# Kernel tuning notes

Measured on AMD Instinct MI355X. Metric: run time of the kernel, lower is better.

The kernel has to match this reference:

```python
import jax, jax.numpy as jnp
import numpy as np

E = 64          # num experts
CAP = 64        # tokens per expert (uniform routing)
H = 1024        # hidden_size
F = 2048        # ffn_hidden_size


def setup_inputs() -> dict:
    key = jax.random.key(0)
    k1, k2, k3 = jax.random.split(key, 3)
    x = jax.random.normal(k1, (E * CAP, H), dtype=jnp.float32)
    # dMoE stores expert weights flattened as [E*F, H]
    w1 = jax.random.normal(k2, (E * F, H), dtype=jnp.float32) * 0.02
    w2 = jax.random.normal(k3, (E * F, H), dtype=jnp.float32) * 0.02
    return {"x": x, "w1": w1, "w2": w2, "num_experts": E}


def reference(x, w1, w2, num_experts):
    # Block-sparse sdd/dsd over a block-diagonal expert topology is a grouped GEMM:
    # tokens are sorted by expert; each group of CAP tokens hits one expert's weights.
    T, Hd = x.shape
    Fd = w1.shape[0] // num_experts
    cap = T // num_experts
    xg = x.reshape(num_experts, cap, Hd)            # [E, cap, H]
    w1g = w1.reshape(num_experts, Fd, Hd)           # [E, F, H]
    w2g = w2.reshape(num_experts, Fd, Hd)           # [E, F, H]
    # sdd: x @ w1^T restricted to expert blocks
    h = jnp.einsum('ech,efh->ecf', xg, w1g)         # [E, cap, F]
    # megablocks' gelu kernel uses the tanh approximation
    h = jax.nn.gelu(h, approximate=True)
    # dsd: h @ w2 restricted to expert blocks
    out = jnp.einsum('ecf,efh->ech', h, w2g)        # [E, cap, H]
    return out.reshape(T, Hd)
```

## Files before the change

### kernel.cpp

```cpp
#include <hip/hip_runtime.h>


typedef __attribute__((ext_vector_type(8))) short short8;
typedef __attribute__((ext_vector_type(4))) float f32x4;
typedef __attribute__((ext_vector_type(8))) unsigned short ushort8;

#define NE   64
#define CAPT 64
#define HD   1024
#define FD   2048

__device__ __forceinline__ unsigned short f2bf(float f) {
  union { float f; unsigned u; } v; v.f = f;
  unsigned r = v.u + 0x7FFFu + ((v.u >> 16) & 1u);
  return (unsigned short)(r >> 16);
}

__device__ __forceinline__ float gelu_t(float v) {
  float u = 1.5957691216057308f * (v + 0.044715f * v * v * v);
  return v / (1.0f + __expf(-u));
}

__device__ __forceinline__ int swz(int row, int kbyte) {
  return row * 128 + (kbyte ^ ((row & 7) << 4));
}
__device__ __forceinline__ int swz2(int row, int kbyte) {
  return row * 256 + (kbyte ^ ((row & 7) << 4));
}

__device__ __forceinline__ void cvt_wr4(unsigned char* dst, f32x4 v) {
  uint2 p;
  p.x = (unsigned)f2bf(v.x) | ((unsigned)f2bf(v.y) << 16);
  p.y = (unsigned)f2bf(v.z) | ((unsigned)f2bf(v.w) << 16);
  *(uint2*)dst = p;
}

__device__ __forceinline__ void tile_barrier() {
  asm volatile("s_waitcnt lgkmcnt(0)" ::: "memory");
  __builtin_amdgcn_s_barrier();
  __builtin_amdgcn_sched_barrier(0);
}

__device__ __forceinline__ int xcd_swz(int bid, int grid) {
  return (bid & 7) * (grid >> 3) + (bid >> 3);
}

#define P1_TSZ (64 * 256)
__global__ __launch_bounds__(512, 4)
void moe_pass1(const float* __restrict__ x, const float* __restrict__ w1,
               unsigned short* __restrict__ hb) {
  __shared__ __align__(16) unsigned char sA[2 * P1_TSZ];
  __shared__ __align__(16) unsigned char sB[2 * P1_TSZ];
  const int bid = xcd_swz(blockIdx.x, NE * 32);
  const int e = bid >> 5, nb = bid & 31;
  const int t = threadIdx.x, lane = t & 63, wid = t >> 6;
  const int wm = wid >> 2, wn = wid & 3;
  const int lr = lane & 15, lk16 = (lane >> 4) * 16;

  const float* xg  = x  + (size_t)e * CAPT * HD;
  const float* w1g = w1 + ((size_t)e * FD + (size_t)nb * 64) * HD;

  f32x4 acc[2] = {};

  f32x4 ra0[4], ra1[4], rb0[4], rb1[4];
  auto loadA = [&](f32x4 (&ra)[4], int k0) {
    #pragma unroll
    for (int i = 0; i < 4; ++i) {
      int u = t + i * 512;
      ra[i] = *(const f32x4*)(xg + (u >> 5) * HD + k0 + (u & 31) * 4);
    }
  };
  auto loadB = [&](f32x4 (&rb)[4], int k0) {
    #pragma unroll
    for (int i = 0; i < 4; ++i) {
      int u = t + i * 512;
      rb[i] = __builtin_nontemporal_load(
          (const f32x4*)(w1g + (u >> 5) * HD + k0 + (u & 31) * 4));
    }
  };
  auto writeT = [&](unsigned char* a, unsigned char* b,
                    f32x4 (&ra)[4], f32x4 (&rb)[4]) {
    #pragma unroll
    for (int i = 0; i < 4; ++i) {
      int u = t + i * 512;
      cvt_wr4(a + swz2(u >> 5, (u & 31) * 8), ra[i]);
    }
    #pragma unroll
    for (int i = 0; i < 4; ++i) {
      int u = t + i * 512;
      cvt_wr4(b + swz2(u >> 5, (u & 31) * 8), rb[i]);
    }
  };

  const int NK = HD / 128;
  loadA(ra0, 0);   loadB(rb0, 0);
  writeT(sA, sB, ra0, rb0);
  loadA(ra1, 128); loadB(rb1, 128);
  loadA(ra0, 256); loadB(rb0, 256);
  tile_barrier();

  int cur = 0;
  auto step = [&](int ks, f32x4 (&raS)[4], f32x4 (&rbS)[4]) {
    unsigned char* cA = sA + cur * P1_TSZ;
    unsigned char* cB = sB + cur * P1_TSZ;
    if (ks + 1 < NK) writeT(sA + (cur ^ 1) * P1_TSZ, sB + (cur ^ 1) * P1_TSZ,
                            raS, rbS);
    if (ks + 3 < NK) { loadA(raS, (ks + 3) * 128); loadB(rbS, (ks + 3) * 128); }

    #pragma unroll
    for (int kk = 0; kk < 4; ++kk) {
      short8 af0 = *(const short8*)(cA + swz2(wm * 32 + lr,      kk * 64 + lk16));
      short8 af1 = *(const short8*)(cA + swz2(wm * 32 + 16 + lr, kk * 64 + lk16));
      short8 bfr = *(const short8*)(cB + swz2(wn * 16 + lr,      kk * 64 + lk16));
      acc[0] = __builtin_amdgcn_mfma_f32_16x16x32_bf16(af0, bfr, acc[0], 0, 0, 0);
      acc[1] = __builtin_amdgcn_mfma_f32_16x16x32_bf16(af1, bfr, acc[1], 0, 0, 0);
    }
    tile_barrier();
    cur ^= 1;
  };
  #pragma unroll 1
  for (int ks = 0; ks < NK; ks += 2) {
    step(ks,     ra1, rb1);
    step(ks + 1, ra0, rb0);
  }

  unsigned short* hp = hb + (size_t)e * CAPT * FD + nb * 64;
  #pragma unroll
  for (int fm = 0; fm < 2; ++fm)
    #pragma unroll
    for (int j = 0; j < 4; ++j) {
      int m = wm * 32 + fm * 16 + (lane >> 4) * 4 + j;
      int f = wn * 16 + lr;
      hp[(size_t)m * FD + f] = f2bf(gelu_t(acc[fm][j]));
    }
}

#define A_SZ (64 * 128)
#define B_SZ (128 * 128)

__global__ __launch_bounds__(512, 4)
void moe_pass2(const unsigned short* __restrict__ hb, const float* __restrict__ w2,
               float* __restrict__ out) {
  __shared__ __align__(16) unsigned char sA[2 * A_SZ];
  __shared__ __align__(16) unsigned char sB[2 * B_SZ];
  const int bid = xcd_swz(blockIdx.x, NE * 8);
  const int e = bid >> 3, nb = bid & 7;
  const int t = threadIdx.x, lane = t & 63, wid = t >> 6;
  const int wm = wid >> 2, wn = wid & 3;
  const int lr = lane & 15, lkb = (lane >> 4) * 16;

  const unsigned short* hg = hb + (size_t)e * CAPT * FD;
  const float* w2g = w2 + (size_t)e * FD * HD + nb * 128;

  f32x4 acc[2][2] = {};

  const int ar = t >> 3, ac = t & 7;
  const int bn = t & 127, bkg = t >> 7;

  ushort8 rav0, rav1;
  float rbv0[16], rbv1[16];
  auto loadA = [&](ushort8& rav, int f0) {
    rav = *(const ushort8*)(hg + (size_t)ar * FD + f0 + ac * 8);
  };
  auto loadB = [&](float (&rbv)[16], int f0) {
    #pragma unroll
    for (int i = 0; i < 4; ++i)
      #pragma unroll
      for (int j = 0; j < 4; ++j)
        rbv[i * 4 + j] = __builtin_nontemporal_load(
            w2g + (size_t)(f0 + bkg * 16 + i * 4 + j) * HD + bn);
  };
  auto writeT = [&](unsigned char* a, unsigned char* b,
                    ushort8& rav, float (&rbv)[16]) {
    *(ushort8*)(a + swz(ar, ac * 16)) = rav;
    #pragma unroll
    for (int i = 0; i < 4; ++i) {
      uint2 p;
      p.x = (unsigned)f2bf(rbv[i * 4 + 0]) | ((unsigned)f2bf(rbv[i * 4 + 1]) << 16);
      p.y = (unsigned)f2bf(rbv[i * 4 + 2]) | ((unsigned)f2bf(rbv[i * 4 + 3]) << 16);
      *(uint2*)(b + swz(bn, (bkg * 16 + i * 4) * 2)) = p;
    }
  };

  const int NK = FD / 64;
  loadA(rav0, 0);   loadB(rbv0, 0);
  writeT(sA, sB, rav0, rbv0);
  loadA(rav1, 64);  loadB(rbv1, 64);
  loadA(rav0, 128); loadB(rbv0, 128);
  tile_barrier();

  int cur = 0;
  auto step = [&](int ks, ushort8& ravS, float (&rbvS)[16]) {
    unsigned char* cA = sA + cur * A_SZ;
    unsigned char* cB = sB + cur * B_SZ;
    if (ks + 1 < NK) writeT(sA + (cur ^ 1) * A_SZ, sB + (cur ^ 1) * B_SZ,
                            ravS, rbvS);
    if (ks + 3 < NK) { loadA(ravS, (ks + 3) * 64); loadB(rbvS, (ks + 3) * 64); }

    short8 af[2][2], bf[2][2];
    #pragma unroll
    for (int fm = 0; fm < 2; ++fm)
      #pragma unroll
      for (int kk = 0; kk < 2; ++kk)
        af[fm][kk] = *(const short8*)(cA + swz(wm * 32 + fm * 16 + lr, kk * 64 + lkb));
    #pragma unroll
    for (int fn = 0; fn < 2; ++fn)
      #pragma unroll
      for (int kk = 0; kk < 2; ++kk)
        bf[fn][kk] = *(const short8*)(cB + swz(wn * 32 + fn * 16 + lr, kk * 64 + lkb));
    #pragma unroll
    for (int fm = 0; fm < 2; ++fm)
      #pragma unroll
      for (int fn = 0; fn < 2; ++fn) {
        acc[fm][fn] = __builtin_amdgcn_mfma_f32_16x16x32_bf16(af[fm][0], bf[fn][0], acc[fm][fn], 0, 0, 0);
        acc[fm][fn] = __builtin_amdgcn_mfma_f32_16x16x32_bf16(af[fm][1], bf[fn][1], acc[fm][fn], 0, 0, 0);
      }
    tile_barrier();
    cur ^= 1;
  };
  #pragma unroll 1
  for (int ks = 0; ks < NK; ks += 2) {
    step(ks,     rav1, rbv1);
    step(ks + 1, rav0, rbv0);
  }

  float* op = out + (size_t)e * CAPT * HD + nb * 128;
  #pragma unroll
  for (int fm = 0; fm < 2; ++fm)
    #pragma unroll
    for (int fn = 0; fn < 2; ++fn)
      #pragma unroll
      for (int j = 0; j < 4; ++j) {
        int m = wm * 32 + fm * 16 + (lane >> 4) * 4 + j;
        int n = wn * 32 + fn * 16 + lr;
        __builtin_nontemporal_store(acc[fm][fn][j], op + (size_t)m * HD + n);
      }
}

extern "C" void kernel_launch(void* const* d_in, const int* in_sizes, int n_in,
                              void* d_out, int out_size, void* d_ws, size_t ws_size,
                              hipStream_t stream) {
  const float* x  = (const float*)d_in[0];
  const float* w1 = (const float*)d_in[1];
  const float* w2 = (const float*)d_in[2];
  float* out = (float*)d_out;
  unsigned short* hb = (unsigned short*)d_ws;
  (void)in_sizes; (void)n_in; (void)out_size; (void)ws_size;

  moe_pass1<<<dim3(NE * (FD / 64)), dim3(512), 0, stream>>>(x, w1, hb);
  moe_pass2<<<dim3(NE * (HD / 128)), dim3(512), 0, stream>>>(hb, w2, out);
}
```

Baseline: 205.7 us.

## Restructure pass1: keep expert x tile in LDS, stream w1 directly into MFMA registers

Pass1 now launches one block per expert quarter (512 F columns). Each block converts the whole 64x1024 x tile to bf16 once into a 128KB LDS buffer. Each wave then loads its own 64 rows of w1 straight from global memory into registers, packs them with v_cvt_pk_bf16_f32, and feeds them to the MFMAs as B fragments, so weights never pass through LDS and the per-step barriers are gone. This removes the repeated x reloads across 32 blocks per expert and the LDS round trip for weights. The cost is a much smaller grid (256 blocks), higher LDS and register use per block, and uncoalesced per-lane w1 loads.

```diff
diff --git a/kernel.cpp b/kernel.cpp
--- a/kernel.cpp
+++ b/kernel.cpp
@@ -3,6 +3,7 @@
 
 typedef __attribute__((ext_vector_type(8))) short short8;
 typedef __attribute__((ext_vector_type(4))) float f32x4;
+typedef __attribute__((ext_vector_type(4))) unsigned int uint4v;
 typedef __attribute__((ext_vector_type(8))) unsigned short ushort8;
 
 #define NE   64
@@ -21,11 +22,19 @@
   return v / (1.0f + __expf(-u));
 }
 
+__device__ __forceinline__ short8 pack_bf16x8(f32x4 a, f32x4 b) {
+  union { uint4v u; short8 s; } r;
+  unsigned d0, d1, d2, d3;
+  asm("v_cvt_pk_bf16_f32 %0,%1,%2" : "=v"(d0) : "v"(a.x), "v"(a.y));
+  asm("v_cvt_pk_bf16_f32 %0,%1,%2" : "=v"(d1) : "v"(a.z), "v"(a.w));
+  asm("v_cvt_pk_bf16_f32 %0,%1,%2" : "=v"(d2) : "v"(b.x), "v"(b.y));
+  asm("v_cvt_pk_bf16_f32 %0,%1,%2" : "=v"(d3) : "v"(b.z), "v"(b.w));
+  r.u.x = d0; r.u.y = d1; r.u.z = d2; r.u.w = d3;
+  return r.s;
+}
+
 __device__ __forceinline__ int swz(int row, int kbyte) {
   return row * 128 + (kbyte ^ ((row & 7) << 4));
-}
-__device__ __forceinline__ int swz2(int row, int kbyte) {
-  return row * 256 + (kbyte ^ ((row & 7) << 4));
 }
 
 __device__ __forceinline__ void cvt_wr4(unsigned char* dst, f32x4 v) {
@@ -45,94 +54,76 @@
   return (bid & 7) * (grid >> 3) + (bid >> 3);
 }
 
-#define P1_TSZ (64 * 256)
-__global__ __launch_bounds__(512, 4)
+__global__ __launch_bounds__(512, 2)
 void moe_pass1(const float* __restrict__ x, const float* __restrict__ w1,
                unsigned short* __restrict__ hb) {
-  __shared__ __align__(16) unsigned char sA[2 * P1_TSZ];
-  __shared__ __align__(16) unsigned char sB[2 * P1_TSZ];
-  const int bid = xcd_swz(blockIdx.x, NE * 32);
-  const int e = bid >> 5, nb = bid & 31;
+  __shared__ __align__(16) unsigned char sX[64 * 2048];
+  const int sb = xcd_swz(blockIdx.x, NE * 4);
+  const int e = sb >> 2, slice = sb & 3;
   const int t = threadIdx.x, lane = t & 63, wid = t >> 6;
-  const int wm = wid >> 2, wn = wid & 3;
-  const int lr = lane & 15, lk16 = (lane >> 4) * 16;
-
-  const float* xg  = x  + (size_t)e * CAPT * HD;
-  const float* w1g = w1 + ((size_t)e * FD + (size_t)nb * 64) * HD;
-
-  f32x4 acc[2] = {};
-
-  f32x4 ra0[4], ra1[4], rb0[4], rb1[4];
-  auto loadA = [&](f32x4 (&ra)[4], int k0) {
-    #pragma unroll
-    for (int i = 0; i < 4; ++i) {
-      int u = t + i * 512;
-      ra[i] = *(const f32x4*)(xg + (u >> 5) * HD + k0 + (u & 31) * 4);
+  const int lr = lane & 15, kg = lane >> 4;
+
+  const float* xg  = x + (size_t)e * CAPT * HD;
+  const float* w1g = w1 + ((size_t)e * FD + (size_t)slice * 512 + wid * 64) * HD;
+
+  #pragma unroll
+  for (int i = 0; i < 32; ++i) {
+    int u = t + i * 512;
+    int r = u >> 8, c = u & 255;
+    f32x4 v = *(const f32x4*)(xg + r * HD + c * 4);
+    cvt_wr4(sX + r * 2048 + ((c * 8) ^ ((r & 7) << 4)), v);
+  }
+  __syncthreads();
+
+  f32x4 acc[4][4] = {};
+
+  f32x4 b0[8], b1[8];
+  auto loadB = [&](f32x4 (&bs)[8], int k0) {
+    #pragma unroll
+    for (int j = 0; j < 4; ++j) {
+      const float* rp = w1g + (size_t)(j * 16 + lr) * HD + k0 + kg * 8;
+      bs[j * 2]     = __builtin_nontemporal_load((const f32x4*)rp);
+      bs[j * 2 + 1] = __builtin_nontemporal_load((const f32x4*)rp + 1);
     }
   };
-  auto loadB = [&](f32x4 (&rb)[4], int k0) {
-    #pragma unroll
-    for (int i = 0; i < 4; ++i) {
-      int u = t + i * 512;
-      rb[i] = __builtin_nontemporal_load(
-          (const f32x4*)(w1g + (u >> 5) * HD + k0 + (u & 31) * 4));
+  auto step = [&](f32x4 (&bs)[8], int ks) {
+    short8 bf[4];
+    #pragma unroll
+    for (int j = 0; j < 4; ++j) bf[j] = pack_bf16x8(bs[j * 2], bs[j * 2 + 1]);
+    if (ks + 2 < 32) loadB(bs, (ks + 2) * 32);
+    short8 af[4];
+    #pragma unroll
+    for (int mt = 0; mt < 4; ++mt) {
+      int row = mt * 16 + lr;
+      af[mt] = *(const short8*)(sX + row * 2048 +
+                                ((ks * 64 + kg * 16) ^ ((row & 7) << 4)));
     }
-  };
-  auto writeT = [&](unsigned char* a, unsigned char* b,
-                    f32x4 (&ra)[4], f32x4 (&rb)[4]) {
-    #pragma unroll
-    for (int i = 0; i < 4; ++i) {
-      int u = t + i * 512;
-      cvt_wr4(a + swz2(u >> 5, (u & 31) * 8), ra[i]);
-    }
-    #pragma unroll
-    for (int i = 0; i < 4; ++i) {
-      int u = t + i * 512;
-      cvt_wr4(b + swz2(u >> 5, (u & 31) * 8), rb[i]);
-    }
-  };
-
-  const int NK = HD / 128;
-  loadA(ra0, 0);   loadB(rb0, 0);
-  writeT(sA, sB, ra0, rb0);
-  loadA(ra1, 128); loadB(rb1, 128);
-  loadA(ra0, 256); loadB(rb0, 256);
-  tile_barrier();
-
-  int cur = 0;
-  auto step = [&](int ks, f32x4 (&raS)[4], f32x4 (&rbS)[4]) {
-    unsigned char* cA = sA + cur * P1_TSZ;
-    unsigned char* cB = sB + cur * P1_TSZ;
-    if (ks + 1 < NK) writeT(sA + (cur ^ 1) * P1_TSZ, sB + (cur ^ 1) * P1_TSZ,
-                            raS, rbS);
-    if (ks + 3 < NK) { loadA(raS, (ks + 3) * 128); loadB(rbS, (ks + 3) * 128); }
-
-    #pragma unroll
-    for (int kk = 0; kk < 4; ++kk) {
-      short8 af0 = *(const short8*)(cA + swz2(wm * 32 + lr,      kk * 64 + lk16));
-      short8 af1 = *(const short8*)(cA + swz2(wm * 32 + 16 + lr, kk * 64 + lk16));
-      short8 bfr = *(const short8*)(cB + swz2(wn * 16 + lr,      kk * 64 + lk16));
-      acc[0] = __builtin_amdgcn_mfma_f32_16x16x32_bf16(af0, bfr, acc[0], 0, 0, 0);
-      acc[1] = __builtin_amdgcn_mfma_f32_16x16x32_bf16(af1, bfr, acc[1], 0, 0, 0);
-    }
-    tile_barrier();
-    cur ^= 1;
-  };
+    #pragma unroll
+    for (int mt = 0; mt < 4; ++mt)
+      #pragma unroll
+      for (int j = 0; j < 4; ++j)
+        acc[mt][j] = __builtin_amdgcn_mfma_f32_16x16x32_bf16(af[mt], bf[j], acc[mt][j], 0, 0, 0);
+  };
+
+  loadB(b0, 0);
+  loadB(b1, 32);
   #pragma unroll 1
-  for (int ks = 0; ks < NK; ks += 2) {
-    step(ks,     ra1, rb1);
-    step(ks + 1, ra0, rb0);
+  for (int ks = 0; ks < 32; ks += 2) {
+    step(b0, ks);
+    step(b1, ks + 1);
   }
 
-  unsigned short* hp = hb + (size_t)e * CAPT * FD + nb * 64;
+  unsigned short* hp = hb + (size_t)e * CAPT * FD + slice * 512 + wid * 64;
   #pragma unroll
-  for (int fm = 0; fm < 2; ++fm)
-    #pragma unroll
-    for (int j = 0; j < 4; ++j) {
-      int m = wm * 32 + fm * 16 + (lane >> 4) * 4 + j;
-      int f = wn * 16 + lr;
-      hp[(size_t)m * FD + f] = f2bf(gelu_t(acc[fm][j]));
-    }
+  for (int mt = 0; mt < 4; ++mt)
+    #pragma unroll
+    for (int j = 0; j < 4; ++j)
+      #pragma unroll
+      for (int jj = 0; jj < 4; ++jj) {
+        int m = mt * 16 + (lane >> 4) * 4 + jj;
+        int f = j * 16 + lr;
+        hp[(size_t)m * FD + f] = f2bf(gelu_t(acc[mt][j][jj]));
+      }
 }
 
 #define A_SZ (64 * 128)
@@ -247,6 +238,6 @@
   unsigned short* hb = (unsigned short*)d_ws;
   (void)in_sizes; (void)n_in; (void)out_size; (void)ws_size;
 
-  moe_pass1<<<dim3(NE * (FD / 64)), dim3(512), 0, stream>>>(x, w1, hb);
-  moe_pass2<<<dim3(NE * (HD / 128)), dim3(512), 0, stream>>>(hb, w2, out);
-}
+  moe_pass1<<<dim3(NE * 4), dim3(512), 0, stream>>>(x, w1, hb);
+  moe_pass2<<<dim3(NE * 8), dim3(512), 0, stream>>>(hb, w2, out);
+}
```

New measurement: 230.8 us. 1.12x slower.
